# Kernel tuning notes

Hardware: AMD Instinct MI355X
Metric: run time of the kernel (lower is better)

## Reference

```python
import jax, jax.numpy as jnp
import numpy as np

B, N, D = 64, 8192, 128
IN, OUT, H = 64, 64, 512
NH_R, NH_W = 4, 4
GD_R = D + 6          # k, beta, g, s(3), gamma
GD_W = 3 * D + 6      # + erase, add
LSTM_IN = IN + OUT + NH_R * D
EPS = 1e-10


def setup_inputs() -> dict:
    key = jax.random.key(0)
    ks = jax.random.split(key, 18)
    f32 = jnp.float32

    def nrm(k, shape, scale=1.0):
        return (jax.random.normal(k, shape) * scale).astype(f32)

    mem_dev = 1.0 / float(np.sqrt(N + D))   # matches NTMMemory.initialize_memory scale
    return {
        'x_input': nrm(ks[0], (B, IN)),
        'prev_y': nrm(ks[1], (B, OUT)),
        'prev_read': nrm(ks[2], (B, NH_R * D), 0.1),
        'memory': nrm(ks[3], (B, N, D), mem_dev),
        'prev_w_read': jax.nn.softmax(nrm(ks[4], (B, NH_R, N)), axis=-1),
        'prev_w_write': jax.nn.softmax(nrm(ks[5], (B, NH_W, N)), axis=-1),
        'h0': nrm(ks[6], (B, H), 0.1),
        'c0': nrm(ks[7], (B, H), 0.1),
        'W_ih': nrm(ks[8], (4 * H, LSTM_IN), 1.0 / np.sqrt(LSTM_IN)),
        'W_hh': nrm(ks[9], (4 * H, H), 1.0 / np.sqrt(H)),
        'b_ih': jnp.zeros((4 * H,), f32),
        'b_hh': jnp.zeros((4 * H,), f32),
        'W_rhead': nrm(ks[10], (NH_R * GD_R, H), 1.0 / np.sqrt(H)),
        'b_rhead': jnp.zeros((NH_R * GD_R,), f32),
        'W_whead': nrm(ks[11], (NH_W * GD_W, H), 1.0 / np.sqrt(H)),
        'b_whead': jnp.zeros((NH_W * GD_W,), f32),
        'W_out': nrm(ks[12], (OUT, H + NH_R * D), 1.0 / np.sqrt(H + NH_R * D)),
        'b_out': jnp.zeros((OUT,), f32),
    }


def _address(ctrl, W, b, nh, gd, memory, prev_w):
    """Content + location addressing for nh heads. ctrl:[B,H] -> w:[B,nh,N]."""
    o = (ctrl @ W.T + b).reshape(ctrl.shape[0], nh, gd)
    k = o[..., :D]                                          # [B,nh,D]
    beta = jax.nn.softplus(o[..., D:D + 1])
    g = jax.nn.sigmoid(o[..., D + 1:D + 2])
    s = jax.nn.softmax(jax.nn.softplus(o[..., D + 2:D + 5]), axis=-1)  # 3-way shift
    gamma = 1.0 + jax.nn.softplus(o[..., D + 5:D + 6])
    # batched cosine similarity (replaces triple python loop in source)
    kn = k / (jnp.linalg.norm(k, axis=-1, keepdims=True) + EPS)
    mn = memory / (jnp.linalg.norm(memory, axis=-1, keepdims=True) + EPS)
    sim = jnp.einsum('bhd,bnd->bhn', kn, mn)                # [B,nh,N]
    wc = jax.nn.softmax(beta * sim, axis=-1)
    # interpolation + circular convolution shift (shifts -1,0,+1)
    wg = g * wc + (1.0 - g) * prev_w
    ws = (s[..., 0:1] * jnp.roll(wg, 1, axis=-1)
          + s[..., 1:2] * wg
          + s[..., 2:3] * jnp.roll(wg, -1, axis=-1))
    # sharpening
    wp = ws ** gamma
    w = wp / (jnp.sum(wp, axis=-1, keepdims=True) + EPS)
    return w, o


def reference(x_input, prev_y, prev_read, memory, prev_w_read, prev_w_write,
              h0, c0, W_ih, W_hh, b_ih, b_hh,
              W_rhead, b_rhead, W_whead, b_whead, W_out, b_out):
    # --- controller: one LSTM step (PyTorch gate order i,f,g,o) ---
    ctrl_in = jnp.concatenate([x_input, prev_y, prev_read], axis=-1)   # [B,LSTM_IN]
    gates = ctrl_in @ W_ih.T + b_ih + h0 @ W_hh.T + b_hh               # [B,4H]
    i, f, gg, o = jnp.split(gates, 4, axis=-1)
    c = jax.nn.sigmoid(f) * c0 + jax.nn.sigmoid(i) * jnp.tanh(gg)
    h = jax.nn.sigmoid(o) * jnp.tanh(c)
    # --- write heads: address then erase/add (batched outer products) ---
    w_w, ow = _address(h, W_whead, b_whead, NH_W, GD_W, memory, prev_w_write)
    erase = ow[..., D + 6:2 * D + 6]       # raw slices, as in source _generate_addressing
    add = ow[..., 2 * D + 6:3 * D + 6]
    mem = memory
    for hidx in range(NH_W):               # small fixed head count
        wv = w_w[:, hidx, :, None]         # [B,N,1]
        mem = mem * (1.0 - wv * erase[:, hidx, None, :]) + wv * add[:, hidx, None, :]
    # --- read heads ---
    w_r, _ = _address(h, W_rhead, b_rhead, NH_R, GD_R, mem, prev_w_read)
    r = jnp.einsum('bhn,bnd->bhd', w_r, mem)                # [B,NH_R,D]
    # --- external output fn ---
    ext_in = jnp.concatenate([h, r.reshape(r.shape[0], NH_R * D)], axis=-1)
    y = jnp.tanh(ext_in @ W_out.T + b_out)                  # [B,OUT]
    return (y, mem, h, c, w_r, w_w)
```

## Files before the change

### kernel.cpp

```cpp
#include <hip/hip_runtime.h>
#include <math.h>

#define B 64
#define N 8192
#define D 128
#define H 512
#define NHEAD 4
#define GDW 390
#define GDR 134
#define KL 1152
#define EPSF 1e-10f

__device__ __forceinline__ float softplusf(float x) {
    return x > 20.f ? x : log1pf(expf(x));
}
__device__ __forceinline__ float sigmoidf(float x) {
    return 1.f / (1.f + expf(-x));
}

__global__ void prep_xt(const float* __restrict__ x, const float* __restrict__ py,
                        const float* __restrict__ pr, const float* __restrict__ h0,
                        float* __restrict__ XT) {
    int idx = blockIdx.x * 256 + threadIdx.x;
    if (idx >= KL * B) return;
    int k = idx >> 6, b = idx & 63;
    float v;
    if (k < 64)       v = x[b * 64 + k];
    else if (k < 128) v = py[b * 64 + (k - 64)];
    else if (k < 640) v = pr[b * 512 + (k - 128)];
    else              v = h0[b * 512 + (k - 640)];
    XT[idx] = v;
}

__global__ __launch_bounds__(256) void controller(const float* __restrict__ XT,
        const float* __restrict__ W_ih, const float* __restrict__ W_hh,
        const float* __restrict__ b_ih, const float* __restrict__ b_hh,
        float* __restrict__ gatesT) {
    __shared__ float xs[64 * 64];
    int tid = threadIdx.x;
    int lane = tid & 63;
    int wave = tid >> 6;
    int j0 = blockIdx.x * 16 + wave * 4;
    float acc[4] = {0.f, 0.f, 0.f, 0.f};
    for (int k0 = 0; k0 < KL; k0 += 64) {
        __syncthreads();
        #pragma unroll
        for (int i = 0; i < 16; i++) xs[tid + i * 256] = XT[k0 * 64 + tid + i * 256];
        __syncthreads();
        const float* wp[4];
        #pragma unroll
        for (int jj = 0; jj < 4; jj++) {
            int j = j0 + jj;
            wp[jj] = (k0 < 640) ? (W_ih + j * 640 + k0) : (W_hh + j * 512 + (k0 - 640));
        }
        #pragma unroll 4
        for (int k = 0; k < 64; k++) {
            float xv = xs[k * 64 + lane];
            #pragma unroll
            for (int jj = 0; jj < 4; jj++) acc[jj] = fmaf(wp[jj][k], xv, acc[jj]);
        }
    }
    #pragma unroll
    for (int jj = 0; jj < 4; jj++) {
        int j = j0 + jj;
        gatesT[j * 64 + lane] = acc[jj] + b_ih[j] + b_hh[j];
    }
}

__global__ void lstm_cell(const float* __restrict__ gatesT, const float* __restrict__ c0,
                          float* __restrict__ h_out, float* __restrict__ c_out,
                          float* __restrict__ HT) {
    int tid = blockIdx.x * 256 + threadIdx.x;
    int b = tid >> 9, u = tid & 511;
    float gi = gatesT[u * 64 + b];
    float gf = gatesT[(512 + u) * 64 + b];
    float gg = gatesT[(1024 + u) * 64 + b];
    float go = gatesT[(1536 + u) * 64 + b];
    float c = sigmoidf(gf) * c0[b * 512 + u] + sigmoidf(gi) * tanhf(gg);
    float h = sigmoidf(go) * tanhf(c);
    c_out[b * 512 + u] = c;
    h_out[b * 512 + u] = h;
    HT[u * 64 + b] = h;
}

__global__ __launch_bounds__(256) void head_proj(const float* __restrict__ HT,
        const float* __restrict__ W_w, const float* __restrict__ W_r,
        const float* __restrict__ b_w, const float* __restrict__ b_r,
        float* __restrict__ o_w, float* __restrict__ o_r) {
    __shared__ float xs[64 * 64];
    int tid = threadIdx.x;
    int lane = tid & 63;
    int wave = tid >> 6;
    int j0 = blockIdx.x * 16 + wave * 4;
    float acc[4] = {0.f, 0.f, 0.f, 0.f};
    const float* wp[4];
    #pragma unroll
    for (int jj = 0; jj < 4; jj++) {
        int j = j0 + jj;
        wp[jj] = (j < 1560) ? (W_w + j * 512) : (W_r + (j - 1560) * 512);
    }
    for (int k0 = 0; k0 < 512; k0 += 64) {
        __syncthreads();
        #pragma unroll
        for (int i = 0; i < 16; i++) xs[tid + i * 256] = HT[k0 * 64 + tid + i * 256];
        __syncthreads();
        #pragma unroll 4
        for (int k = 0; k < 64; k++) {
            float xv = xs[k * 64 + lane];
            #pragma unroll
            for (int jj = 0; jj < 4; jj++) acc[jj] = fmaf(wp[jj][k0 + k], xv, acc[jj]);
        }
    }
    #pragma unroll
    for (int jj = 0; jj < 4; jj++) {
        int j = j0 + jj;
        if (j < 1560) o_w[lane * 1560 + j] = acc[jj] + b_w[j];
        else          o_r[lane * 536 + (j - 1560)] = acc[jj] + b_r[j - 1560];
    }
}

__global__ __launch_bounds__(128) void head_params(const float* __restrict__ o_w,
        const float* __restrict__ o_r, float* __restrict__ knw, float* __restrict__ knr,
        float* __restrict__ pw, float* __restrict__ prd) {
    __shared__ float red[2];
    int id = blockIdx.x;
    bool isw = id < 256;
    int bh = isw ? id : id - 256;
    const float* o = isw ? (o_w + (bh >> 2) * 1560 + (bh & 3) * GDW)
                         : (o_r + (bh >> 2) * 536 + (bh & 3) * GDR);
    float* kn = (isw ? knw : knr) + bh * 128;
    float* pp = (isw ? pw : prd) + bh * 6;
    int t = threadIdx.x;
    float kv = o[t];
    float ss = kv * kv;
    #pragma unroll
    for (int m = 1; m < 64; m <<= 1) ss += __shfl_xor(ss, m);
    if ((t & 63) == 0) red[t >> 6] = ss;
    __syncthreads();
    float norm = sqrtf(red[0] + red[1]);
    kn[t] = kv / (norm + EPSF);
    if (t == 0) {
        float beta = softplusf(o[128]);
        float g = sigmoidf(o[129]);
        float s0 = softplusf(o[130]), s1 = softplusf(o[131]), s2 = softplusf(o[132]);
        float mx = fmaxf(s0, fmaxf(s1, s2));
        float e0 = expf(s0 - mx), e1 = expf(s1 - mx), e2 = expf(s2 - mx);
        float inv = 1.f / (e0 + e1 + e2);
        float gamma = 1.f + softplusf(o[133]);
        pp[0] = beta; pp[1] = g; pp[2] = e0 * inv; pp[3] = e1 * inv; pp[4] = e2 * inv; pp[5] = gamma;
    }
}

__global__ __launch_bounds__(256) void sim_write(const float* __restrict__ mem,
        const float* __restrict__ knw, float* __restrict__ sim) {
    int t = threadIdx.x;
    int l = t & 31;
    int rg = t >> 5;
    int b = blockIdx.x >> 7;
    int n0 = (blockIdx.x & 127) * 64;
    const float4 k0 = *(const float4*)(knw + (b * 4 + 0) * 128 + l * 4);
    const float4 k1 = *(const float4*)(knw + (b * 4 + 1) * 128 + l * 4);
    const float4 k2 = *(const float4*)(knw + (b * 4 + 2) * 128 + l * 4);
    const float4 k3 = *(const float4*)(knw + (b * 4 + 3) * 128 + l * 4);
    for (int it = 0; it < 8; it++) {
        int n = n0 + it * 8 + rg;
        const float4 m = *(const float4*)(mem + ((size_t)b * N + n) * D + l * 4);
        float s0 = m.x * k0.x + m.y * k0.y + m.z * k0.z + m.w * k0.w;
        float s1 = m.x * k1.x + m.y * k1.y + m.z * k1.z + m.w * k1.w;
        float s2 = m.x * k2.x + m.y * k2.y + m.z * k2.z + m.w * k2.w;
        float s3 = m.x * k3.x + m.y * k3.y + m.z * k3.z + m.w * k3.w;
        float nn = m.x * m.x + m.y * m.y + m.z * m.z + m.w * m.w;
        #pragma unroll
        for (int msk = 1; msk < 32; msk <<= 1) {
            s0 += __shfl_xor(s0, msk);
            s1 += __shfl_xor(s1, msk);
            s2 += __shfl_xor(s2, msk);
            s3 += __shfl_xor(s3, msk);
            nn += __shfl_xor(nn, msk);
        }
        if (l < 4) {
            float dv = (l == 0) ? s0 : (l == 1) ? s1 : (l == 2) ? s2 : s3;
            sim[((size_t)(b * 4 + l)) * N + n] = dv / (sqrtf(nn) + EPSF);
        }
    }
}

__global__ __launch_bounds__(256) void addr_finalize(const float* __restrict__ sim,
        const float* __restrict__ prev_w, const float* __restrict__ par,
        float* __restrict__ w_out) {
    __shared__ float buf[N];
    __shared__ float red[4];
    int bh = blockIdx.x;
    int t = threadIdx.x;
    const float* s = sim + (size_t)bh * N;
    const float* pw = prev_w + (size_t)bh * N;
    float beta = par[bh * 6 + 0], g = par[bh * 6 + 1];
    float s0 = par[bh * 6 + 2], s1 = par[bh * 6 + 3], s2 = par[bh * 6 + 4];
    float gamma = par[bh * 6 + 5];
    float mx = -INFINITY;
    for (int i = t; i < N; i += 256) {
        float e = beta * s[i];
        buf[i] = e;
        mx = fmaxf(mx, e);
    }
    #pragma unroll
    for (int m = 1; m < 64; m <<= 1) mx = fmaxf(mx, __shfl_xor(mx, m));
    if ((t & 63) == 0) red[t >> 6] = mx;
    __syncthreads();
    mx = fmaxf(fmaxf(red[0], red[1]), fmaxf(red[2], red[3]));
    float sum = 0.f;
    for (int i = t; i < N; i += 256) {
        float v = expf(buf[i] - mx);
        buf[i] = v;
        sum += v;
    }
    #pragma unroll
    for (int m = 1; m < 64; m <<= 1) sum += __shfl_xor(sum, m);
    __syncthreads();
    if ((t & 63) == 0) red[t >> 6] = sum;
    __syncthreads();
    sum = red[0] + red[1] + red[2] + red[3];
    float inv = 1.f / sum;
    for (int i = t; i < N; i += 256) buf[i] = g * (buf[i] * inv) + (1.f - g) * pw[i];
    __syncthreads();
    float psum = 0.f;
    for (int i = t; i < N; i += 256) {
        float wsv = s0 * buf[(i + N - 1) & (N - 1)] + s1 * buf[i] + s2 * buf[(i + 1) & (N - 1)];
        psum += powf(wsv, gamma);
    }
    #pragma unroll
    for (int m = 1; m < 64; m <<= 1) psum += __shfl_xor(psum, m);
    __syncthreads();
    if ((t & 63) == 0) red[t >> 6] = psum;
    __syncthreads();
    psum = red[0] + red[1] + red[2] + red[3];
    float rinv = 1.f / (psum + EPSF);
    for (int i = t; i < N; i += 256) {
        float wsv = s0 * buf[(i + N - 1) & (N - 1)] + s1 * buf[i] + s2 * buf[(i + 1) & (N - 1)];
        w_out[(size_t)bh * N + i] = powf(wsv, gamma) * rinv;
    }
}

__global__ __launch_bounds__(256) void mem_update(const float* __restrict__ mem_in,
        const float* __restrict__ o_w, const float* __restrict__ w_w,
        const float* __restrict__ knr, float* __restrict__ mem_out,
        float* __restrict__ simr) {
    int t = threadIdx.x;
    int l = t & 31;
    int rg = t >> 5;
    int b = blockIdx.x >> 7;
    int n0 = (blockIdx.x & 127) * 64;
    float4 e[4], a[4], kr[4];
    #pragma unroll
    for (int h = 0; h < 4; h++) {
        const float* ob = o_w + b * 1560 + h * GDW;
        e[h].x = ob[134 + l * 4 + 0]; e[h].y = ob[134 + l * 4 + 1];
        e[h].z = ob[134 + l * 4 + 2]; e[h].w = ob[134 + l * 4 + 3];
        a[h].x = ob[262 + l * 4 + 0]; a[h].y = ob[262 + l * 4 + 1];
        a[h].z = ob[262 + l * 4 + 2]; a[h].w = ob[262 + l * 4 + 3];
        kr[h] = *(const float4*)(knr + (b * 4 + h) * 128 + l * 4);
    }
    for (int it = 0; it < 8; it++) {
        int n = n0 + it * 8 + rg;
        size_t base = ((size_t)b * N + n) * D + l * 4;
        float4 m = *(const float4*)(mem_in + base);
        #pragma unroll
        for (int h = 0; h < 4; h++) {
            float wv = w_w[((size_t)(b * 4 + h)) * N + n];
            m.x = m.x * (1.f - wv * e[h].x) + wv * a[h].x;
            m.y = m.y * (1.f - wv * e[h].y) + wv * a[h].y;
            m.z = m.z * (1.f - wv * e[h].z) + wv * a[h].z;
            m.w = m.w * (1.f - wv * e[h].w) + wv * a[h].w;
        }
        *(float4*)(mem_out + base) = m;
        float s0 = m.x * kr[0].x + m.y * kr[0].y + m.z * kr[0].z + m.w * kr[0].w;
        float s1 = m.x * kr[1].x + m.y * kr[1].y + m.z * kr[1].z + m.w * kr[1].w;
        float s2 = m.x * kr[2].x + m.y * kr[2].y + m.z * kr[2].z + m.w * kr[2].w;
        float s3 = m.x * kr[3].x + m.y * kr[3].y + m.z * kr[3].z + m.w * kr[3].w;
        float nn = m.x * m.x + m.y * m.y + m.z * m.z + m.w * m.w;
        #pragma unroll
        for (int msk = 1; msk < 32; msk <<= 1) {
            s0 += __shfl_xor(s0, msk);
            s1 += __shfl_xor(s1, msk);
            s2 += __shfl_xor(s2, msk);
            s3 += __shfl_xor(s3, msk);
            nn += __shfl_xor(nn, msk);
        }
        if (l < 4) {
            float dv = (l == 0) ? s0 : (l == 1) ? s1 : (l == 2) ? s2 : s3;
            simr[((size_t)(b * 4 + l)) * N + n] = dv / (sqrtf(nn) + EPSF);
        }
    }
}

__global__ void zero_r(float* __restrict__ r) {
    r[blockIdx.x * 256 + threadIdx.x] = 0.f;
}

__global__ __launch_bounds__(256) void read_vec(const float* __restrict__ mem,
        const float* __restrict__ w_r, float* __restrict__ r) {
    __shared__ float lds[8 * 512];
    int t = threadIdx.x;
    int l = t & 31;
    int rg = t >> 5;
    int b = blockIdx.x >> 4;
    int n0 = (blockIdx.x & 15) * 512;
    float4 acc[4];
    #pragma unroll
    for (int h = 0; h < 4; h++) acc[h] = make_float4(0.f, 0.f, 0.f, 0.f);
    for (int it = 0; it < 64; it++) {
        int n = n0 + it * 8 + rg;
        const float4 m = *(const float4*)(mem + ((size_t)b * N + n) * D + l * 4);
        #pragma unroll
        for (int h = 0; h < 4; h++) {
            float wv = w_r[((size_t)(b * 4 + h)) * N + n];
            acc[h].x += wv * m.x;
            acc[h].y += wv * m.y;
            acc[h].z += wv * m.z;
            acc[h].w += wv * m.w;
        }
    }
    #pragma unroll
    for (int h = 0; h < 4; h++) *(float4*)(lds + rg * 512 + h * 128 + l * 4) = acc[h];
    __syncthreads();
    for (int o = t; o < 512; o += 256) {
        float sum = 0.f;
        #pragma unroll
        for (int g2 = 0; g2 < 8; g2++) sum += lds[g2 * 512 + o];
        atomicAdd(&r[b * 512 + o], sum);
    }
}

__global__ __launch_bounds__(64) void out_y(const float* __restrict__ h,
        const float* __restrict__ r, const float* __restrict__ W_out,
        const float* __restrict__ b_out, float* __restrict__ y) {
    int b = blockIdx.x >> 6;
    int j = blockIdx.x & 63;
    int l = threadIdx.x;
    float acc = 0.f;
    #pragma unroll
    for (int kk = 0; kk < 16; kk++) {
        int k = l + kk * 64;
        float x = (k < 512) ? h[b * 512 + k] : r[b * 512 + (k - 512)];
        acc = fmaf(W_out[j * 1024 + k], x, acc);
    }
    #pragma unroll
    for (int m = 1; m < 64; m <<= 1) acc += __shfl_xor(acc, m);
    if (l == 0) y[b * 64 + j] = tanhf(acc + b_out[j]);
}

extern "C" void kernel_launch(void* const* d_in, const int* in_sizes, int n_in,
                              void* d_out, int out_size, void* d_ws, size_t ws_size,
                              hipStream_t stream) {
    const float* x_input      = (const float*)d_in[0];
    const float* prev_y       = (const float*)d_in[1];
    const float* prev_read    = (const float*)d_in[2];
    const float* memory       = (const float*)d_in[3];
    const float* prev_w_read  = (const float*)d_in[4];
    const float* prev_w_write = (const float*)d_in[5];
    const float* h0           = (const float*)d_in[6];
    const float* c0           = (const float*)d_in[7];
    const float* W_ih         = (const float*)d_in[8];
    const float* W_hh         = (const float*)d_in[9];
    const float* b_ih         = (const float*)d_in[10];
    const float* b_hh         = (const float*)d_in[11];
    const float* W_rhead      = (const float*)d_in[12];
    const float* b_rhead      = (const float*)d_in[13];
    const float* W_whead      = (const float*)d_in[14];
    const float* b_whead      = (const float*)d_in[15];
    const float* W_out        = (const float*)d_in[16];
    const float* b_out        = (const float*)d_in[17];

    float* out = (float*)d_out;
    float* y_o   = out;
    float* mem_o = out + 4096;
    float* h_o   = out + 4096 + 67108864;
    float* c_o   = h_o + 32768;
    float* wr_o  = c_o + 32768;
    float* ww_o  = wr_o + 2097152;

    float* ws     = (float*)d_ws;
    float* XT     = ws;
    float* HT     = XT + 73728;
    float* gatesT = HT + 32768;
    float* o_w    = gatesT + 131072;
    float* o_r    = o_w + 99840;
    float* knw    = o_r + 34304;
    float* knr    = knw + 32768;
    float* pw     = knr + 32768;
    float* prd    = pw + 1536;
    float* sim_w  = prd + 1536;
    float* sim_r  = sim_w + 2097152;
    float* r_ws   = sim_r + 2097152;

    prep_xt<<<288, 256, 0, stream>>>(x_input, prev_y, prev_read, h0, XT);
    controller<<<128, 256, 0, stream>>>(XT, W_ih, W_hh, b_ih, b_hh, gatesT);
    lstm_cell<<<128, 256, 0, stream>>>(gatesT, c0, h_o, c_o, HT);
    head_proj<<<131, 256, 0, stream>>>(HT, W_whead, W_rhead, b_whead, b_rhead, o_w, o_r);
    head_params<<<512, 128, 0, stream>>>(o_w, o_r, knw, knr, pw, prd);
    sim_write<<<8192, 256, 0, stream>>>(memory, knw, sim_w);
    addr_finalize<<<256, 256, 0, stream>>>(sim_w, prev_w_write, pw, ww_o);
    mem_update<<<8192, 256, 0, stream>>>(memory, o_w, ww_o, knr, mem_o, sim_r);
    addr_finalize<<<256, 256, 0, stream>>>(sim_r, prev_w_read, prd, wr_o);
    zero_r<<<128, 256, 0, stream>>>(r_ws);
    read_vec<<<1024, 256, 0, stream>>>(mem_o, wr_o, r_ws);
    out_y<<<4096, 64, 0, stream>>>(h_o, r_ws, W_out, b_out, y_o);
}
```

Before: 824.1 us.

## Tighten reductions, cache weights in LDS, fold zeroing, widen addressing blocks

The sim_write and mem_update kernels switch from full 5-value butterfly reductions to transpose-style reductions that fold the four head dots and the norm into fewer shuffles. mem_update and read_vec stage the per-row head weights into LDS instead of reading them from global memory inside the loop. addr_finalize runs with 512 threads and caches the powf results in shared memory so it does not recompute them. The zero_r launch is folded into head_params. This trims shuffle and ALU overhead and one kernel launch, at the cost of more LDS per block in addr_finalize (64KB), which may limit occupancy.

After: 756.5 us. 1.09x faster.

```diff
diff --git a/kernel.cpp b/kernel.cpp
--- a/kernel.cpp
+++ b/kernel.cpp
@@ -121,9 +121,10 @@
 
 __global__ __launch_bounds__(128) void head_params(const float* __restrict__ o_w,
         const float* __restrict__ o_r, float* __restrict__ knw, float* __restrict__ knr,
-        float* __restrict__ pw, float* __restrict__ prd) {
+        float* __restrict__ pw, float* __restrict__ prd, float* __restrict__ rzero) {
     __shared__ float red[2];
     int id = blockIdx.x;
+    if (id < 256) rzero[id * 128 + threadIdx.x] = 0.f;
     bool isw = id < 256;
     int bh = isw ? id : id - 256;
     const float* o = isw ? (o_w + (bh >> 2) * 1560 + (bh & 3) * GDW)
@@ -154,42 +155,53 @@
 __global__ __launch_bounds__(256) void sim_write(const float* __restrict__ mem,
         const float* __restrict__ knw, float* __restrict__ sim) {
     int t = threadIdx.x;
-    int l = t & 31;
-    int rg = t >> 5;
+    int lane = t & 63;
+    int wv = t >> 6;
+    int j = lane & 15;
+    int u = lane >> 4;
     int b = blockIdx.x >> 7;
-    int n0 = (blockIdx.x & 127) * 64;
-    const float4 k0 = *(const float4*)(knw + (b * 4 + 0) * 128 + l * 4);
-    const float4 k1 = *(const float4*)(knw + (b * 4 + 1) * 128 + l * 4);
-    const float4 k2 = *(const float4*)(knw + (b * 4 + 2) * 128 + l * 4);
-    const float4 k3 = *(const float4*)(knw + (b * 4 + 3) * 128 + l * 4);
-    for (int it = 0; it < 8; it++) {
-        int n = n0 + it * 8 + rg;
-        const float4 m = *(const float4*)(mem + ((size_t)b * N + n) * D + l * 4);
-        float s0 = m.x * k0.x + m.y * k0.y + m.z * k0.z + m.w * k0.w;
-        float s1 = m.x * k1.x + m.y * k1.y + m.z * k1.z + m.w * k1.w;
-        float s2 = m.x * k2.x + m.y * k2.y + m.z * k2.z + m.w * k2.w;
-        float s3 = m.x * k3.x + m.y * k3.y + m.z * k3.z + m.w * k3.w;
-        float nn = m.x * m.x + m.y * m.y + m.z * m.z + m.w * m.w;
-        #pragma unroll
-        for (int msk = 1; msk < 32; msk <<= 1) {
-            s0 += __shfl_xor(s0, msk);
-            s1 += __shfl_xor(s1, msk);
-            s2 += __shfl_xor(s2, msk);
-            s3 += __shfl_xor(s3, msk);
-            nn += __shfl_xor(nn, msk);
-        }
-        if (l < 4) {
-            float dv = (l == 0) ? s0 : (l == 1) ? s1 : (l == 2) ? s2 : s3;
-            sim[((size_t)(b * 4 + l)) * N + n] = dv / (sqrtf(nn) + EPSF);
-        }
-    }
-}
-
-__global__ __launch_bounds__(256) void addr_finalize(const float* __restrict__ sim,
+    int nb = (blockIdx.x & 127) * 64 + wv * 16 + u;
+    float4 k[4][2];
+    #pragma unroll
+    for (int h = 0; h < 4; h++) {
+        #pragma unroll
+        for (int s = 0; s < 2; s++)
+            k[h][s] = *(const float4*)(knw + (b * 4 + h) * 128 + s * 64 + j * 4);
+    }
+    #pragma unroll
+    for (int it = 0; it < 4; it++) {
+        int n = nb + it * 4;
+        size_t base = ((size_t)b * N + n) * D + j * 4;
+        const float4 m0 = *(const float4*)(mem + base);
+        const float4 m1 = *(const float4*)(mem + base + 64);
+        float s0 = m0.x*k[0][0].x + m0.y*k[0][0].y + m0.z*k[0][0].z + m0.w*k[0][0].w
+                 + m1.x*k[0][1].x + m1.y*k[0][1].y + m1.z*k[0][1].z + m1.w*k[0][1].w;
+        float s1 = m0.x*k[1][0].x + m0.y*k[1][0].y + m0.z*k[1][0].z + m0.w*k[1][0].w
+                 + m1.x*k[1][1].x + m1.y*k[1][1].y + m1.z*k[1][1].z + m1.w*k[1][1].w;
+        float s2 = m0.x*k[2][0].x + m0.y*k[2][0].y + m0.z*k[2][0].z + m0.w*k[2][0].w
+                 + m1.x*k[2][1].x + m1.y*k[2][1].y + m1.z*k[2][1].z + m1.w*k[2][1].w;
+        float s3 = m0.x*k[3][0].x + m0.y*k[3][0].y + m0.z*k[3][0].z + m0.w*k[3][0].w
+                 + m1.x*k[3][1].x + m1.y*k[3][1].y + m1.z*k[3][1].z + m1.w*k[3][1].w;
+        float nn = m0.x*m0.x + m0.y*m0.y + m0.z*m0.z + m0.w*m0.w
+                 + m1.x*m1.x + m1.y*m1.y + m1.z*m1.z + m1.w*m1.w;
+        s0 += __shfl_xor(s0, 1); s1 += __shfl_xor(s1, 1);
+        s2 += __shfl_xor(s2, 1); s3 += __shfl_xor(s3, 1); nn += __shfl_xor(nn, 1);
+        float p01 = (j & 1) ? s1 : s0;
+        float p23 = (j & 1) ? s3 : s2;
+        p01 += __shfl_xor(p01, 2); p23 += __shfl_xor(p23, 2); nn += __shfl_xor(nn, 2);
+        float q = (j & 2) ? p23 : p01;
+        q += __shfl_xor(q, 4);  nn += __shfl_xor(nn, 4);
+        q += __shfl_xor(q, 8);  nn += __shfl_xor(nn, 8);
+        if (j < 4) sim[((size_t)(b * 4 + j)) * N + n] = q / (sqrtf(nn) + EPSF);
+    }
+}
+
+__global__ __launch_bounds__(512) void addr_finalize(const float* __restrict__ sim,
         const float* __restrict__ prev_w, const float* __restrict__ par,
         float* __restrict__ w_out) {
     __shared__ float buf[N];
-    __shared__ float red[4];
+    __shared__ float pbuf[N];
+    __shared__ float red[8];
     int bh = blockIdx.x;
     int t = threadIdx.x;
     const float* s = sim + (size_t)bh * N;
@@ -198,7 +210,7 @@
     float s0 = par[bh * 6 + 2], s1 = par[bh * 6 + 3], s2 = par[bh * 6 + 4];
     float gamma = par[bh * 6 + 5];
     float mx = -INFINITY;
-    for (int i = t; i < N; i += 256) {
+    for (int i = t; i < N; i += 512) {
         float e = beta * s[i];
         buf[i] = e;
         mx = fmaxf(mx, e);
@@ -207,9 +219,11 @@
     for (int m = 1; m < 64; m <<= 1) mx = fmaxf(mx, __shfl_xor(mx, m));
     if ((t & 63) == 0) red[t >> 6] = mx;
     __syncthreads();
-    mx = fmaxf(fmaxf(red[0], red[1]), fmaxf(red[2], red[3]));
+    mx = red[0];
+    #pragma unroll
+    for (int kk = 1; kk < 8; kk++) mx = fmaxf(mx, red[kk]);
     float sum = 0.f;
-    for (int i = t; i < N; i += 256) {
+    for (int i = t; i < N; i += 512) {
         float v = expf(buf[i] - mx);
         buf[i] = v;
         sum += v;
@@ -219,37 +233,41 @@
     __syncthreads();
     if ((t & 63) == 0) red[t >> 6] = sum;
     __syncthreads();
-    sum = red[0] + red[1] + red[2] + red[3];
+    sum = red[0] + red[1] + red[2] + red[3] + red[4] + red[5] + red[6] + red[7];
     float inv = 1.f / sum;
-    for (int i = t; i < N; i += 256) buf[i] = g * (buf[i] * inv) + (1.f - g) * pw[i];
+    for (int i = t; i < N; i += 512) buf[i] = g * (buf[i] * inv) + (1.f - g) * pw[i];
     __syncthreads();
     float psum = 0.f;
-    for (int i = t; i < N; i += 256) {
+    for (int i = t; i < N; i += 512) {
         float wsv = s0 * buf[(i + N - 1) & (N - 1)] + s1 * buf[i] + s2 * buf[(i + 1) & (N - 1)];
-        psum += powf(wsv, gamma);
+        float pv = powf(wsv, gamma);
+        pbuf[i] = pv;
+        psum += pv;
     }
     #pragma unroll
     for (int m = 1; m < 64; m <<= 1) psum += __shfl_xor(psum, m);
     __syncthreads();
     if ((t & 63) == 0) red[t >> 6] = psum;
     __syncthreads();
-    psum = red[0] + red[1] + red[2] + red[3];
+    psum = red[0] + red[1] + red[2] + red[3] + red[4] + red[5] + red[6] + red[7];
     float rinv = 1.f / (psum + EPSF);
-    for (int i = t; i < N; i += 256) {
-        float wsv = s0 * buf[(i + N - 1) & (N - 1)] + s1 * buf[i] + s2 * buf[(i + 1) & (N - 1)];
-        w_out[(size_t)bh * N + i] = powf(wsv, gamma) * rinv;
-    }
+    for (int i = t; i < N; i += 512) w_out[(size_t)bh * N + i] = pbuf[i] * rinv;
 }
 
 __global__ __launch_bounds__(256) void mem_update(const float* __restrict__ mem_in,
         const float* __restrict__ o_w, const float* __restrict__ w_w,
         const float* __restrict__ knr, float* __restrict__ mem_out,
         float* __restrict__ simr) {
+    __shared__ float wlds[4][64];
     int t = threadIdx.x;
     int l = t & 31;
     int rg = t >> 5;
     int b = blockIdx.x >> 7;
     int n0 = (blockIdx.x & 127) * 64;
+    {
+        int h = t >> 6, idx = t & 63;
+        wlds[h][idx] = w_w[((size_t)(b * 4 + h)) * N + n0 + idx];
+    }
     float4 e[4], a[4], kr[4];
     #pragma unroll
     for (int h = 0; h < 4; h++) {
@@ -260,13 +278,14 @@
         a[h].z = ob[262 + l * 4 + 2]; a[h].w = ob[262 + l * 4 + 3];
         kr[h] = *(const float4*)(knr + (b * 4 + h) * 128 + l * 4);
     }
+    __syncthreads();
     for (int it = 0; it < 8; it++) {
         int n = n0 + it * 8 + rg;
         size_t base = ((size_t)b * N + n) * D + l * 4;
         float4 m = *(const float4*)(mem_in + base);
         #pragma unroll
         for (int h = 0; h < 4; h++) {
-            float wv = w_w[((size_t)(b * 4 + h)) * N + n];
+            float wv = wlds[h][it * 8 + rg];
             m.x = m.x * (1.f - wv * e[h].x) + wv * a[h].x;
             m.y = m.y * (1.f - wv * e[h].y) + wv * a[h].y;
             m.z = m.z * (1.f - wv * e[h].z) + wv * a[h].z;
@@ -278,42 +297,44 @@
         float s2 = m.x * kr[2].x + m.y * kr[2].y + m.z * kr[2].z + m.w * kr[2].w;
         float s3 = m.x * kr[3].x + m.y * kr[3].y + m.z * kr[3].z + m.w * kr[3].w;
         float nn = m.x * m.x + m.y * m.y + m.z * m.z + m.w * m.w;
-        #pragma unroll
-        for (int msk = 1; msk < 32; msk <<= 1) {
-            s0 += __shfl_xor(s0, msk);
-            s1 += __shfl_xor(s1, msk);
-            s2 += __shfl_xor(s2, msk);
-            s3 += __shfl_xor(s3, msk);
-            nn += __shfl_xor(nn, msk);
-        }
-        if (l < 4) {
-            float dv = (l == 0) ? s0 : (l == 1) ? s1 : (l == 2) ? s2 : s3;
-            simr[((size_t)(b * 4 + l)) * N + n] = dv / (sqrtf(nn) + EPSF);
-        }
-    }
-}
-
-__global__ void zero_r(float* __restrict__ r) {
-    r[blockIdx.x * 256 + threadIdx.x] = 0.f;
+        s0 += __shfl_xor(s0, 1); s1 += __shfl_xor(s1, 1);
+        s2 += __shfl_xor(s2, 1); s3 += __shfl_xor(s3, 1); nn += __shfl_xor(nn, 1);
+        float p01 = (l & 1) ? s1 : s0;
+        float p23 = (l & 1) ? s3 : s2;
+        p01 += __shfl_xor(p01, 2); p23 += __shfl_xor(p23, 2); nn += __shfl_xor(nn, 2);
+        float q = (l & 2) ? p23 : p01;
+        q += __shfl_xor(q, 4); nn += __shfl_xor(nn, 4);
+        float z = (l & 4) ? nn : q;
+        z += __shfl_xor(z, 8);
+        z += __shfl_xor(z, 16);
+        float nnv = __shfl_xor(z, 4);
+        if (l < 4) simr[((size_t)(b * 4 + l)) * N + n] = z / (sqrtf(nnv) + EPSF);
+    }
 }
 
 __global__ __launch_bounds__(256) void read_vec(const float* __restrict__ mem,
         const float* __restrict__ w_r, float* __restrict__ r) {
     __shared__ float lds[8 * 512];
+    __shared__ float wlds[4][512];
     int t = threadIdx.x;
     int l = t & 31;
     int rg = t >> 5;
     int b = blockIdx.x >> 4;
     int n0 = (blockIdx.x & 15) * 512;
+    for (int i = t; i < 2048; i += 256) {
+        int h = i >> 9, idx = i & 511;
+        wlds[h][idx] = w_r[((size_t)(b * 4 + h)) * N + n0 + idx];
+    }
+    __syncthreads();
     float4 acc[4];
     #pragma unroll
     for (int h = 0; h < 4; h++) acc[h] = make_float4(0.f, 0.f, 0.f, 0.f);
     for (int it = 0; it < 64; it++) {
-        int n = n0 + it * 8 + rg;
-        const float4 m = *(const float4*)(mem + ((size_t)b * N + n) * D + l * 4);
+        int nl = it * 8 + rg;
+        const float4 m = *(const float4*)(mem + ((size_t)b * N + n0 + nl) * D + l * 4);
         #pragma unroll
         for (int h = 0; h < 4; h++) {
-            float wv = w_r[((size_t)(b * 4 + h)) * N + n];
+            float wv = wlds[h][nl];
             acc[h].x += wv * m.x;
             acc[h].y += wv * m.y;
             acc[h].z += wv * m.z;
@@ -397,12 +418,11 @@
     controller<<<128, 256, 0, stream>>>(XT, W_ih, W_hh, b_ih, b_hh, gatesT);
     lstm_cell<<<128, 256, 0, stream>>>(gatesT, c0, h_o, c_o, HT);
     head_proj<<<131, 256, 0, stream>>>(HT, W_whead, W_rhead, b_whead, b_rhead, o_w, o_r);
-    head_params<<<512, 128, 0, stream>>>(o_w, o_r, knw, knr, pw, prd);
+    head_params<<<512, 128, 0, stream>>>(o_w, o_r, knw, knr, pw, prd, r_ws);
     sim_write<<<8192, 256, 0, stream>>>(memory, knw, sim_w);
-    addr_finalize<<<256, 256, 0, stream>>>(sim_w, prev_w_write, pw, ww_o);
+    addr_finalize<<<256, 512, 0, stream>>>(sim_w, prev_w_write, pw, ww_o);
     mem_update<<<8192, 256, 0, stream>>>(memory, o_w, ww_o, knr, mem_o, sim_r);
-    addr_finalize<<<256, 256, 0, stream>>>(sim_r, prev_w_read, prd, wr_o);
-    zero_r<<<128, 256, 0, stream>>>(r_ws);
+    addr_finalize<<<256, 512, 0, stream>>>(sim_r, prev_w_read, prd, wr_o);
     read_vec<<<1024, 256, 0, stream>>>(mem_o, wr_o, r_ws);
     out_y<<<4096, 64, 0, stream>>>(h_o, r_ws, W_out, b_out, y_o);
 }
```
